# Kernel optimization log

Hardware: AMD Instinct MI355X
Metric: run time of the kernel (lower is better)

Reference implementation:

```python
import jax, jax.numpy as jnp
import numpy as np

B, T, D = 16, 4096, 1024
UNITS = 1024


def setup_inputs() -> dict:
    key = jax.random.key(0)
    ks = jax.random.split(key, 8)
    s_in = 1.0 / np.sqrt(D)
    s_u = 1.0 / np.sqrt(UNITS)
    return {
        "hidden_state": jax.random.normal(ks[0], (B, D), jnp.float32),
        "encoder_output": jax.random.normal(ks[1], (B, T, D), jnp.float32),
        "W1": jax.random.normal(ks[2], (D, UNITS), jnp.float32) * s_in,
        "b1": jnp.zeros((UNITS,), jnp.float32),
        "W2": jax.random.normal(ks[3], (D, UNITS), jnp.float32) * s_in,
        "b2": jnp.zeros((UNITS,), jnp.float32),
        "V": jax.random.normal(ks[4], (UNITS, 1), jnp.float32) * s_u,
        "bv": jnp.zeros((1,), jnp.float32),
    }


def reference(hidden_state, encoder_output, W1, b1, W2, b2, V, bv):
    # Bahdanau additive attention: score = V(tanh(W1(h) + W2(enc)))
    h_proj = hidden_state @ W1 + b1                      # [B, U]
    e_proj = jnp.einsum("btd,du->btu", encoder_output, W2) + b2  # [B, T, U]
    feat = jnp.tanh(h_proj[:, None, :] + e_proj)          # [B, T, U]
    score = feat @ V + bv                                 # [B, T, 1]
    attention_weights = jax.nn.softmax(score, axis=1)     # [B, T, 1]
    context_vector = jnp.sum(attention_weights * encoder_output, axis=1)  # [B, D]
    return context_vector, attention_weights
```

## Files before the change

### kernel.cpp

```cpp
#include <hip/hip_runtime.h>
#include <hip/hip_bf16.h>
#include <math.h>

#define B_ 16
#define T_ 4096
#define D_ 1024
#define U_ 1024
#define M_ (B_*T_)

typedef __attribute__((ext_vector_type(8))) short short8;
typedef __attribute__((ext_vector_type(4))) short short4v;
typedef __attribute__((ext_vector_type(4))) float float4v;

static __device__ __forceinline__ short f2bf(float f) {
    unsigned u = __builtin_bit_cast(unsigned, f);
    u += 0x7FFFu + ((u >> 16) & 1u);
    return (short)(u >> 16);
}
static __device__ __forceinline__ float fast_tanh(float x) {
    float c = fminf(fmaxf(2.f * x, -30.f), 30.f);
    float t = __expf(c);
    return __fdividef(t - 1.f, t + 1.f);
}

#define GLLDS(GP, LP) __builtin_amdgcn_global_load_lds( \
    (const __attribute__((address_space(1))) void*)(GP), \
    (__attribute__((address_space(3))) void*)(LP), 16, 0, 0)

__global__ void prep_fused(const float* __restrict__ h, const float* __restrict__ W1,
                           const float* __restrict__ b1, const float* __restrict__ b2,
                           const float* __restrict__ W2,
                           float* __restrict__ hbp, short* __restrict__ W2T) {
    int bx = blockIdx.x;
    if (bx < 256) {
        int kc = bx >> 6;
        int gid = (bx & 63) * 256 + threadIdx.x;
        int b = gid >> 10, u = gid & 1023;
        const float* hr = h + b * D_ + kc * 256;
        const float* w = W1 + (size_t)(kc * 256) * U_ + u;
        float s0 = 0.f, s1 = 0.f, s2 = 0.f, s3 = 0.f;
        for (int k = 0; k < 256; k += 4) {
            s0 += hr[k+0] * w[(size_t)(k+0) * U_];
            s1 += hr[k+1] * w[(size_t)(k+1) * U_];
            s2 += hr[k+2] * w[(size_t)(k+2) * U_];
            s3 += hr[k+3] * w[(size_t)(k+3) * U_];
        }
        float s = ((s0 + s1) + (s2 + s3));
        if (kc == 0) s += b1[u] + b2[u];
        hbp[kc * 16384 + gid] = s;
    } else {
        __shared__ short t[64][65];
        int x = bx - 256;
        int k0 = (x >> 4) * 64, u0 = (x & 15) * 64;
        int tx = threadIdx.x & 63, ty = threadIdx.x >> 6;
        #pragma unroll
        for (int r = 0; r < 16; ++r) {
            int kk = ty * 16 + r;
            t[kk][tx] = f2bf(W2[(size_t)(k0 + kk) * U_ + u0 + tx]);
        }
        __syncthreads();
        #pragma unroll
        for (int r = 0; r < 16; ++r) {
            int uu = ty * 16 + r;
            W2T[(size_t)(u0 + uu) * D_ + k0 + tx] = t[tx][uu];
        }
    }
}

__global__ __launch_bounds__(512, 2) void gemm_score_8ph(
    const float* __restrict__ encf,
    const short* __restrict__ W2T,
    const float* __restrict__ hbp,
    const float* __restrict__ V,
    float* __restrict__ scorepart)
{
    __shared__ __align__(16) short lds[65536];

    const int tid = threadIdx.x;
    const int g = blockIdx.x;
    const int c = g & 7, q = g >> 3;
    const int ntile = q & 3;
    const int mtile = (q >> 2) * 8 + c;
    const int row0 = mtile * 256, n0 = ntile * 256;
    const int bidx = row0 >> 12;

    const int lane = tid & 63;
    const int wv = tid >> 6;
    const int wm = wv >> 2, wn = wv & 3;
    const int lm = lane & 15, quad = lane >> 4;

    const int srow = tid >> 3;
    const int lslot = (tid & 7) ^ (srow & 7);
    const float* Aenc = encf + (size_t)(row0 + srow) * D_ + lslot * 8;
    const short* bS = W2T + (size_t)(n0 + srow) * D_ + lslot * 8;
    short* bD = lds + 32768 + tid * 8;

#define STG_B(kt, h, bf) do { \
    GLLDS(bS + (size_t)((h) * 128) * D_ + (kt) * 64,      bD + (bf) * 16384 + (h) * 8192); \
    GLLDS(bS + (size_t)((h) * 128 + 64) * D_ + (kt) * 64, bD + (bf) * 16384 + (h) * 8192 + 4096); \
} while (0)
#define LDA_ISSUE(R, kt, hh) do { \
    const float* _p0 = Aenc + (size_t)((hh) * 128) * D_ + (kt) * 64; \
    const float* _p1 = _p0 + (size_t)64 * D_; \
    R##0 = *(const float4v*)_p0; \
    R##1 = *(const float4v*)(_p0 + 4); \
    R##2 = *(const float4v*)_p1; \
    R##3 = *(const float4v*)(_p1 + 4); \
} while (0)
#define LDA_WRITE(R, hh, bfi) do { \
    short8 _w0, _w1; \
    _w0[0]=f2bf(R##0[0]); _w0[1]=f2bf(R##0[1]); _w0[2]=f2bf(R##0[2]); _w0[3]=f2bf(R##0[3]); \
    _w0[4]=f2bf(R##1[0]); _w0[5]=f2bf(R##1[1]); _w0[6]=f2bf(R##1[2]); _w0[7]=f2bf(R##1[3]); \
    _w1[0]=f2bf(R##2[0]); _w1[1]=f2bf(R##2[1]); _w1[2]=f2bf(R##2[2]); _w1[3]=f2bf(R##2[3]); \
    _w1[4]=f2bf(R##3[0]); _w1[5]=f2bf(R##3[1]); _w1[6]=f2bf(R##3[2]); _w1[7]=f2bf(R##3[3]); \
    *(short8*)(lds + (bfi) * 16384 + (hh) * 8192 + tid * 8) = _w0; \
    *(short8*)(lds + (bfi) * 16384 + (hh) * 8192 + 4096 + tid * 8) = _w1; \
} while (0)
#define LDS_RD(off) (*(const short8*)(lds + (off)))
#define MFMA(a, b, c) __builtin_amdgcn_mfma_f32_16x16x32_bf16((a), (b), (c), 0, 0, 0)

    const int aB0 = (wm * 128 + lm) * 64 + (quad ^ (lm & 7)) * 8;
    const int aB1 = aB0 ^ 32;
    const int bB0 = 32768 + (wn * 64 + lm) * 64 + (quad ^ (lm & 7)) * 8;
    const int bB1 = bB0 ^ 32;

    float4v acc[8][4] = {};
    short8 Af[4][2], Bf[4][2];
    float4v rLO0, rLO1, rLO2, rLO3;
    float4v rHI0, rHI1, rHI2, rHI3;

    STG_B(0, 0, 0); STG_B(0, 1, 0);
    LDA_ISSUE(rLO, 0, 0); LDA_ISSUE(rHI, 0, 1);
    STG_B(1, 0, 1); STG_B(1, 1, 1);
    LDA_WRITE(rLO, 0, 0);
    LDA_WRITE(rHI, 1, 0);
    LDA_ISSUE(rLO, 1, 0);
    asm volatile("s_waitcnt lgkmcnt(0)" ::: "memory");
    __builtin_amdgcn_s_barrier();
    __builtin_amdgcn_sched_barrier(0);

    for (int t = 0; t < 16; ++t) {
        const int buf = t & 1;
        const int ab = buf * 16384;
        #pragma unroll
        for (int mi = 0; mi < 4; ++mi) {
            Af[mi][0] = LDS_RD(ab + aB0 + mi * 1024);
            Af[mi][1] = LDS_RD(ab + aB1 + mi * 1024);
        }
        #pragma unroll
        for (int ni = 0; ni < 2; ++ni) {
            Bf[ni][0] = LDS_RD(ab + bB0 + ni * 1024);
            Bf[ni][1] = LDS_RD(ab + bB1 + ni * 1024);
        }
        if (t < 15) LDA_ISSUE(rHI, t + 1, 1);
        __builtin_amdgcn_s_barrier();
        __builtin_amdgcn_s_setprio(1);
        #pragma unroll
        for (int mi = 0; mi < 4; ++mi)
            #pragma unroll
            for (int ni = 0; ni < 2; ++ni) {
                acc[mi][ni] = MFMA(Af[mi][0], Bf[ni][0], acc[mi][ni]);
                acc[mi][ni] = MFMA(Af[mi][1], Bf[ni][1], acc[mi][ni]);
            }
        __builtin_amdgcn_s_setprio(0);
        __builtin_amdgcn_s_barrier();
        #pragma unroll
        for (int ni = 0; ni < 2; ++ni) {
            Bf[2 + ni][0] = LDS_RD(ab + bB0 + (2 + ni) * 1024);
            Bf[2 + ni][1] = LDS_RD(ab + bB1 + (2 + ni) * 1024);
        }
        __builtin_amdgcn_s_barrier();
        __builtin_amdgcn_s_setprio(1);
        #pragma unroll
        for (int mi = 0; mi < 4; ++mi)
            #pragma unroll
            for (int ni = 0; ni < 2; ++ni) {
                acc[mi][2 + ni] = MFMA(Af[mi][0], Bf[2 + ni][0], acc[mi][2 + ni]);
                acc[mi][2 + ni] = MFMA(Af[mi][1], Bf[2 + ni][1], acc[mi][2 + ni]);
            }
        __builtin_amdgcn_s_setprio(0);
        __builtin_amdgcn_s_barrier();
        #pragma unroll
        for (int mi = 0; mi < 4; ++mi) {
            Af[mi][0] = LDS_RD(ab + aB0 + 4096 + mi * 1024);
            Af[mi][1] = LDS_RD(ab + aB1 + 4096 + mi * 1024);
        }
        if (t < 14) STG_B(t + 2, 0, buf);
        __builtin_amdgcn_s_barrier();
        __builtin_amdgcn_s_setprio(1);
        #pragma unroll
        for (int mi = 0; mi < 4; ++mi)
            #pragma unroll
            for (int ni = 0; ni < 2; ++ni) {
                acc[4 + mi][ni] = MFMA(Af[mi][0], Bf[ni][0], acc[4 + mi][ni]);
                acc[4 + mi][ni] = MFMA(Af[mi][1], Bf[ni][1], acc[4 + mi][ni]);
            }
        __builtin_amdgcn_s_setprio(0);
        __builtin_amdgcn_s_barrier();
        if (t < 15) LDA_WRITE(rLO, 0, (t + 1) & 1);
        if (t < 14) { LDA_ISSUE(rLO, t + 2, 0); STG_B(t + 2, 1, buf); }
        if (t < 15) LDA_WRITE(rHI, 1, (t + 1) & 1);
        __builtin_amdgcn_s_barrier();
        __builtin_amdgcn_s_setprio(1);
        #pragma unroll
        for (int mi = 0; mi < 4; ++mi)
            #pragma unroll
            for (int ni = 0; ni < 2; ++ni) {
                acc[4 + mi][2 + ni] = MFMA(Af[mi][0], Bf[2 + ni][0], acc[4 + mi][2 + ni]);
                acc[4 + mi][2 + ni] = MFMA(Af[mi][1], Bf[2 + ni][1], acc[4 + mi][2 + ni]);
            }
        __builtin_amdgcn_s_setprio(0);
        asm volatile("s_waitcnt lgkmcnt(0)" ::: "memory");
        __builtin_amdgcn_s_barrier();
        __builtin_amdgcn_sched_barrier(0);
    }

    float* sbuf = (float*)lds;
    float hbv[4], Vv[4];
    #pragma unroll
    for (int ni = 0; ni < 4; ++ni) {
        int U = n0 + wn * 64 + ni * 16 + lm;
        int o = bidx * U_ + U;
        hbv[ni] = hbp[o] + hbp[16384 + o] + hbp[32768 + o] + hbp[49152 + o];
        Vv[ni]  = V[U];
    }
    #pragma unroll
    for (int mi = 0; mi < 8; ++mi) {
        #pragma unroll
        for (int r = 0; r < 4; ++r) {
            float s = 0.f;
            #pragma unroll
            for (int ni = 0; ni < 4; ++ni)
                s += fast_tanh(acc[mi][ni][r] + hbv[ni]) * Vv[ni];
            #pragma unroll
            for (int off = 1; off < 16; off <<= 1)
                s += __shfl_xor(s, off, 64);
            if (lm == 0)
                sbuf[wn * 256 + wm * 128 + mi * 16 + quad * 4 + r] = s;
        }
    }
    __syncthreads();
    if (tid < 256)
        scorepart[(size_t)ntile * M_ + row0 + tid] =
            sbuf[tid] + sbuf[256 + tid] + sbuf[512 + tid] + sbuf[768 + tid];
}

__global__ __launch_bounds__(256) void ctx_softmax(
        const float* __restrict__ scorepart,
        const float* __restrict__ bv,
        const float* __restrict__ enc,
        float* __restrict__ out_attn,
        float* __restrict__ part)
{
    __shared__ float sm[T_];
    __shared__ float wsm[128];
    __shared__ float lacc[1024];
    __shared__ float red[8];
    const int x = blockIdx.x, tid = threadIdx.x;
    const int b = x & 15, tc = x >> 4;
    const int wvi = tid >> 6;
    const float bv0 = bv[0];
    float lmax = -1e30f;
    #pragma unroll
    for (int i = 0; i < 16; ++i) {
        int t = tid + i * 256;
        const float* sp = scorepart + (size_t)b * T_ + t;
        float s = bv0 + sp[0] + sp[M_] + sp[2 * (size_t)M_] + sp[3 * (size_t)M_];
        sm[t] = s;
        lmax = fmaxf(lmax, s);
    }
    #pragma unroll
    for (int off = 1; off < 64; off <<= 1) lmax = fmaxf(lmax, __shfl_xor(lmax, off, 64));
    if ((tid & 63) == 0) red[wvi] = lmax;
    __syncthreads();
    const float m = fmaxf(fmaxf(red[0], red[1]), fmaxf(red[2], red[3]));
    float lsum = 0.f;
    #pragma unroll
    for (int i = 0; i < 16; ++i) lsum += __expf(sm[tid + i * 256] - m);
    #pragma unroll
    for (int off = 1; off < 64; off <<= 1) lsum += __shfl_xor(lsum, off, 64);
    if ((tid & 63) == 0) red[4 + wvi] = lsum;
    __syncthreads();
    const float tot = (red[4] + red[5]) + (red[6] + red[7]);
    const float rinv = 1.f / tot;
    if ((tid >> 7) == (tc & 1)) {
        int j = tid & 127;
        int t = tc * 128 + j;
        float w = __expf(sm[t] - m) * rinv;
        wsm[j] = w;
        out_attn[b * T_ + t] = w;
    }
    __syncthreads();
    const int par = tid >> 7;
    const int d0 = (tid & 127) * 8;
    const float* e0 = enc + (size_t)(b * T_ + tc * 128 + par) * D_ + d0;
    float4v a0 = {}, a1 = {};
    #pragma unroll 4
    for (int it = 0; it < 64; ++it) {
        float4v v0 = *(const float4v*)(e0 + (size_t)it * 2 * D_);
        float4v v1 = *(const float4v*)(e0 + (size_t)it * 2 * D_ + 4);
        float w = wsm[it * 2 + par];
        a0[0] += w * v0[0]; a0[1] += w * v0[1];
        a0[2] += w * v0[2]; a0[3] += w * v0[3];
        a1[0] += w * v1[0]; a1[1] += w * v1[1];
        a1[2] += w * v1[2]; a1[3] += w * v1[3];
    }
    if (par) {
        *(float4v*)(lacc + (tid & 127) * 8)     = a0;
        *(float4v*)(lacc + (tid & 127) * 8 + 4) = a1;
    }
    __syncthreads();
    if (!par) {
        const float* l = lacc + tid * 8;
        a0[0] += l[0]; a0[1] += l[1]; a0[2] += l[2]; a0[3] += l[3];
        a1[0] += l[4]; a1[1] += l[5]; a1[2] += l[6]; a1[3] += l[7];
        float4v* pp = (float4v*)(part + (size_t)x * 1024 + tid * 8);
        pp[0] = a0; pp[1] = a1;
    }
}

__global__ void ctx_reduce_kernel(const float* __restrict__ part, float* __restrict__ ctx) {
    int gid = blockIdx.x * 256 + threadIdx.x;
    int b = gid >> 10, d = gid & 1023;
    float s = 0.f;
    #pragma unroll
    for (int tc = 0; tc < 32; ++tc) s += part[(size_t)(tc * 16 + b) * 1024 + d];
    ctx[gid] = s;
}

extern "C" void kernel_launch(void* const* d_in, const int* in_sizes, int n_in,
                              void* d_out, int out_size, void* d_ws, size_t ws_size,
                              hipStream_t stream) {
    const float* h   = (const float*)d_in[0];
    const float* enc = (const float*)d_in[1];
    const float* W1  = (const float*)d_in[2];
    const float* b1  = (const float*)d_in[3];
    const float* W2  = (const float*)d_in[4];
    const float* b2  = (const float*)d_in[5];
    const float* V   = (const float*)d_in[6];
    const float* bv  = (const float*)d_in[7];
    float* out = (float*)d_out;
    float* ws  = (float*)d_ws;

    float* hbp       = ws;
    float* scorepart = ws + 65536;
    short* W2T   = (short*)(ws + 65536 + 524288);
    float* ctxpart   = (float*)W2T;

    prep_fused<<<512, 256, 0, stream>>>(h, W1, b1, b2, W2, hbp, W2T);
    gemm_score_8ph<<<1024, 512, 0, stream>>>(enc, W2T, hbp, V, scorepart);
    ctx_softmax<<<512, 256, 0, stream>>>(scorepart, bv, enc, out + 16384, ctxpart);
    ctx_reduce_kernel<<<64, 256, 0, stream>>>(ctxpart, out);
}
```

Measured before the change: 560.5 us.

## Stage fp32 encoder tiles directly into LDS and convert to bf16 at fragment load

Replaces the register-staged A path (global load to VGPRs, bf16 conversion, LDS write) with direct global-to-LDS async copies of the raw fp32 encoder rows in 64-row chunks. The bf16 conversion moves to the point where each wave reads its MFMA fragments from LDS. The aim is to free VGPRs and take the conversion and LDS writes off the staging path, and it adds vmcnt-based waits. In exchange, A now has a single fp32 buffer, so LDS traffic per fragment doubles and every wave (wn=0..3) repeats the same conversions. The rounding also switches to the HIP intrinsic.

```diff
diff --git a/kernel.cpp b/kernel.cpp
--- a/kernel.cpp
+++ b/kernel.cpp
@@ -16,6 +16,16 @@
     unsigned u = __builtin_bit_cast(unsigned, f);
     u += 0x7FFFu + ((u >> 16) & 1u);
     return (short)(u >> 16);
+}
+static __device__ __forceinline__ short bfc(float f) {
+    __hip_bfloat16 b = __float2bfloat16(f);
+    return (short)__builtin_bit_cast(unsigned short, b);
+}
+static __device__ __forceinline__ short8 cvt8(float4v lo, float4v hi) {
+    short8 r;
+    r[0]=bfc(lo[0]); r[1]=bfc(lo[1]); r[2]=bfc(lo[2]); r[3]=bfc(lo[3]);
+    r[4]=bfc(hi[0]); r[5]=bfc(hi[1]); r[6]=bfc(hi[2]); r[7]=bfc(hi[3]);
+    return r;
 }
 static __device__ __forceinline__ float fast_tanh(float x) {
     float c = fminf(fmaxf(2.f * x, -30.f), 30.f);
@@ -89,70 +99,61 @@
     const int wm = wv >> 2, wn = wv & 3;
     const int lm = lane & 15, quad = lane >> 4;
 
-    const int srow = tid >> 3;
-    const int lslot = (tid & 7) ^ (srow & 7);
-    const float* Aenc = encf + (size_t)(row0 + srow) * D_ + lslot * 8;
-    const short* bS = W2T + (size_t)(n0 + srow) * D_ + lslot * 8;
+    const int srow32 = tid >> 4;
+    const int scol = ((((tid & 15) >> 1) ^ (srow32 & 7)) << 3) + ((tid & 1) << 2);
+    const float* aSrc = encf + (size_t)(row0 + srow32) * D_ + scol;
+    char* aDst = (char*)lds + tid * 16;
+
+#define STG_A32(kt, R) do { \
+    GLLDS(aSrc + (size_t)(R) * D_ + (kt) * 64,        aDst + (R) * 256); \
+    GLLDS(aSrc + (size_t)((R) + 32) * D_ + (kt) * 64, aDst + (R) * 256 + 8192); \
+} while (0)
+
+    const int srowB = tid >> 3;
+    const int lslotB = (tid & 7) ^ (srowB & 7);
+    const short* bS = W2T + (size_t)(n0 + srowB) * D_ + lslotB * 8;
     short* bD = lds + 32768 + tid * 8;
-
 #define STG_B(kt, h, bf) do { \
     GLLDS(bS + (size_t)((h) * 128) * D_ + (kt) * 64,      bD + (bf) * 16384 + (h) * 8192); \
     GLLDS(bS + (size_t)((h) * 128 + 64) * D_ + (kt) * 64, bD + (bf) * 16384 + (h) * 8192 + 4096); \
 } while (0)
-#define LDA_ISSUE(R, kt, hh) do { \
-    const float* _p0 = Aenc + (size_t)((hh) * 128) * D_ + (kt) * 64; \
-    const float* _p1 = _p0 + (size_t)64 * D_; \
-    R##0 = *(const float4v*)_p0; \
-    R##1 = *(const float4v*)(_p0 + 4); \
-    R##2 = *(const float4v*)_p1; \
-    R##3 = *(const float4v*)(_p1 + 4); \
-} while (0)
-#define LDA_WRITE(R, hh, bfi) do { \
-    short8 _w0, _w1; \
-    _w0[0]=f2bf(R##0[0]); _w0[1]=f2bf(R##0[1]); _w0[2]=f2bf(R##0[2]); _w0[3]=f2bf(R##0[3]); \
-    _w0[4]=f2bf(R##1[0]); _w0[5]=f2bf(R##1[1]); _w0[6]=f2bf(R##1[2]); _w0[7]=f2bf(R##1[3]); \
-    _w1[0]=f2bf(R##2[0]); _w1[1]=f2bf(R##2[1]); _w1[2]=f2bf(R##2[2]); _w1[3]=f2bf(R##2[3]); \
-    _w1[4]=f2bf(R##3[0]); _w1[5]=f2bf(R##3[1]); _w1[6]=f2bf(R##3[2]); _w1[7]=f2bf(R##3[3]); \
-    *(short8*)(lds + (bfi) * 16384 + (hh) * 8192 + tid * 8) = _w0; \
-    *(short8*)(lds + (bfi) * 16384 + (hh) * 8192 + 4096 + tid * 8) = _w1; \
-} while (0)
 #define LDS_RD(off) (*(const short8*)(lds + (off)))
 #define MFMA(a, b, c) __builtin_amdgcn_mfma_f32_16x16x32_bf16((a), (b), (c), 0, 0, 0)
-
-    const int aB0 = (wm * 128 + lm) * 64 + (quad ^ (lm & 7)) * 8;
-    const int aB1 = aB0 ^ 32;
+#define LDA_FRAG(d0, d1, rw) do { \
+    const int _r = (rw); \
+    const int _p0 = _r * 256 + ((quad ^ (_r & 7)) << 5); \
+    const int _p1 = _r * 256 + (((quad + 4) ^ (_r & 7)) << 5); \
+    float4v _a = *(const float4v*)((const char*)lds + _p0); \
+    float4v _b = *(const float4v*)((const char*)lds + _p0 + 16); \
+    float4v _c = *(const float4v*)((const char*)lds + _p1); \
+    float4v _d = *(const float4v*)((const char*)lds + _p1 + 16); \
+    d0 = cvt8(_a, _b); d1 = cvt8(_c, _d); \
+} while (0)
+
     const int bB0 = 32768 + (wn * 64 + lm) * 64 + (quad ^ (lm & 7)) * 8;
     const int bB1 = bB0 ^ 32;
 
     float4v acc[8][4] = {};
     short8 Af[4][2], Bf[4][2];
-    float4v rLO0, rLO1, rLO2, rLO3;
-    float4v rHI0, rHI1, rHI2, rHI3;
 
     STG_B(0, 0, 0); STG_B(0, 1, 0);
-    LDA_ISSUE(rLO, 0, 0); LDA_ISSUE(rHI, 0, 1);
+    STG_A32(0, 0); STG_A32(0, 128);
+    STG_A32(0, 64); STG_A32(0, 192);
     STG_B(1, 0, 1); STG_B(1, 1, 1);
-    LDA_WRITE(rLO, 0, 0);
-    LDA_WRITE(rHI, 1, 0);
-    LDA_ISSUE(rLO, 1, 0);
-    asm volatile("s_waitcnt lgkmcnt(0)" ::: "memory");
+    asm volatile("s_waitcnt vmcnt(8)" ::: "memory");
     __builtin_amdgcn_s_barrier();
     __builtin_amdgcn_sched_barrier(0);
 
     for (int t = 0; t < 16; ++t) {
-        const int buf = t & 1;
-        const int ab = buf * 16384;
-        #pragma unroll
-        for (int mi = 0; mi < 4; ++mi) {
-            Af[mi][0] = LDS_RD(ab + aB0 + mi * 1024);
-            Af[mi][1] = LDS_RD(ab + aB1 + mi * 1024);
-        }
+        const int bufS = (t & 1) * 16384;
+        #pragma unroll
+        for (int mi = 0; mi < 4; ++mi)
+            LDA_FRAG(Af[mi][0], Af[mi][1], wm * 128 + mi * 16 + lm);
         #pragma unroll
         for (int ni = 0; ni < 2; ++ni) {
-            Bf[ni][0] = LDS_RD(ab + bB0 + ni * 1024);
-            Bf[ni][1] = LDS_RD(ab + bB1 + ni * 1024);
-        }
-        if (t < 15) LDA_ISSUE(rHI, t + 1, 1);
+            Bf[ni][0] = LDS_RD(bufS + bB0 + ni * 1024);
+            Bf[ni][1] = LDS_RD(bufS + bB1 + ni * 1024);
+        }
         __builtin_amdgcn_s_barrier();
         __builtin_amdgcn_s_setprio(1);
         #pragma unroll
@@ -166,9 +167,10 @@
         __builtin_amdgcn_s_barrier();
         #pragma unroll
         for (int ni = 0; ni < 2; ++ni) {
-            Bf[2 + ni][0] = LDS_RD(ab + bB0 + (2 + ni) * 1024);
-            Bf[2 + ni][1] = LDS_RD(ab + bB1 + (2 + ni) * 1024);
-        }
+            Bf[2 + ni][0] = LDS_RD(bufS + bB0 + (2 + ni) * 1024);
+            Bf[2 + ni][1] = LDS_RD(bufS + bB1 + (2 + ni) * 1024);
+        }
+        if (t < 15) { STG_A32(t + 1, 0); STG_A32(t + 1, 128); }
         __builtin_amdgcn_s_barrier();
         __builtin_amdgcn_s_setprio(1);
         #pragma unroll
@@ -179,13 +181,13 @@
                 acc[mi][2 + ni] = MFMA(Af[mi][1], Bf[2 + ni][1], acc[mi][2 + ni]);
             }
         __builtin_amdgcn_s_setprio(0);
-        __builtin_amdgcn_s_barrier();
-        #pragma unroll
-        for (int mi = 0; mi < 4; ++mi) {
-            Af[mi][0] = LDS_RD(ab + aB0 + 4096 + mi * 1024);
-            Af[mi][1] = LDS_RD(ab + aB1 + 4096 + mi * 1024);
-        }
-        if (t < 14) STG_B(t + 2, 0, buf);
+        if (t < 15) { asm volatile("s_waitcnt vmcnt(6)" ::: "memory"); }
+        else        { asm volatile("s_waitcnt vmcnt(0)" ::: "memory"); }
+        __builtin_amdgcn_s_barrier();
+        #pragma unroll
+        for (int mi = 0; mi < 4; ++mi)
+            LDA_FRAG(Af[mi][0], Af[mi][1], wm * 128 + 64 + mi * 16 + lm);
+        if (t < 14) STG_B(t + 2, 0, t & 1);
         __builtin_amdgcn_s_barrier();
         __builtin_amdgcn_s_setprio(1);
         #pragma unroll
@@ -197,9 +199,8 @@
             }
         __builtin_amdgcn_s_setprio(0);
         __builtin_amdgcn_s_barrier();
-        if (t < 15) LDA_WRITE(rLO, 0, (t + 1) & 1);
-        if (t < 14) { LDA_ISSUE(rLO, t + 2, 0); STG_B(t + 2, 1, buf); }
-        if (t < 15) LDA_WRITE(rHI, 1, (t + 1) & 1);
+        if (t < 15) { STG_A32(t + 1, 64); STG_A32(t + 1, 192); }
+        if (t < 14) STG_B(t + 2, 1, t & 1);
         __builtin_amdgcn_s_barrier();
         __builtin_amdgcn_s_setprio(1);
         #pragma unroll
@@ -210,7 +211,8 @@
                 acc[4 + mi][2 + ni] = MFMA(Af[mi][1], Bf[2 + ni][1], acc[4 + mi][2 + ni]);
             }
         __builtin_amdgcn_s_setprio(0);
-        asm volatile("s_waitcnt lgkmcnt(0)" ::: "memory");
+        if (t < 14)      { asm volatile("s_waitcnt vmcnt(8)" ::: "memory"); }
+        else if (t == 14){ asm volatile("s_waitcnt vmcnt(4)" ::: "memory"); }
         __builtin_amdgcn_s_barrier();
         __builtin_amdgcn_sched_barrier(0);
     }
```

Result: no change. 561.7 us (+0.2%).
